# Kernel optimization log

Hardware: AMD Instinct MI355X
Metric: run time of the kernel (lower is better)

Reference implementation:

```python
import jax, jax.numpy as jnp
import numpy as np

D_MODEL, D_K, D_V = 1024, 64, 64
B, S = 4, 4096

def setup_inputs() -> dict:
    key = jax.random.key(0)
    ks = jax.random.split(key, 9)
    s_in = 1.0 / np.sqrt(D_MODEL)
    return {
        "Q": jax.random.normal(ks[0], (B, S, D_MODEL), jnp.float32),
        "K": jax.random.normal(ks[1], (B, S, D_MODEL), jnp.float32),
        "V": jax.random.normal(ks[2], (B, S, D_MODEL), jnp.float32),
        "Wq": jax.random.uniform(ks[3], (D_MODEL, D_K), jnp.float32, -s_in, s_in),
        "bq": jax.random.uniform(ks[4], (D_K,), jnp.float32, -s_in, s_in),
        "Wk": jax.random.uniform(ks[5], (D_MODEL, D_K), jnp.float32, -s_in, s_in),
        "bk": jax.random.uniform(ks[6], (D_K,), jnp.float32, -s_in, s_in),
        "Wv": jax.random.uniform(ks[7], (D_MODEL, D_V), jnp.float32, -s_in, s_in),
        "bv": jax.random.uniform(ks[8], (D_V,), jnp.float32, -s_in, s_in),
    }

def reference(Q, K, V, Wq, bq, Wk, bk, Wv, bv):
    # Linear projections: [B,S,d_model] -> [B,S,d_k/d_v]
    q = jnp.einsum("bsm,mk->bsk", Q, Wq) + bq
    k = jnp.einsum("btm,mk->btk", K, Wk) + bk
    v = jnp.einsum("btm,mv->btv", V, Wv) + bv
    # Scaled dot-product attention, softmax over key axis (dim=2)
    scores = jnp.einsum("bsk,btk->bst", q, k) / jnp.sqrt(jnp.float32(D_K))
    attn = jax.nn.softmax(scores, axis=2)  # [B,S,S]
    return jnp.einsum("bst,btv->bsv", attn, v)
```

## Files before the change

### kernel.cpp

```cpp
#include <hip/hip_runtime.h>

typedef __bf16 bf16;
typedef __attribute__((ext_vector_type(4))) __bf16 bf16x4;
typedef __attribute__((ext_vector_type(8))) __bf16 bf16x8;
typedef __attribute__((ext_vector_type(4))) float f32x4;
typedef __attribute__((ext_vector_type(16))) float f32x16;

#define MFMA16(a, b, c) __builtin_amdgcn_mfma_f32_16x16x32_bf16((a), (b), (c), 0, 0, 0)
#define MFMA32(a, b, c) __builtin_amdgcn_mfma_f32_32x32x16_bf16((a), (b), (c), 0, 0, 0)

typedef __attribute__((address_space(3))) unsigned int lds_u32_t;
typedef __attribute__((address_space(1))) unsigned int glb_u32_t;

__device__ __forceinline__ void gl2lds16(const void* g, void* l) {
    __builtin_amdgcn_global_load_lds((const glb_u32_t*)g, (lds_u32_t*)l, 16, 0, 0);
}

__device__ __forceinline__ bf16 tobf(float f) {
    unsigned u = __float_as_uint(f);
    u += 0x7fffu + ((u >> 16) & 1u);
    unsigned short h = (unsigned short)(u >> 16);
    bf16 r;
    __builtin_memcpy(&r, &h, 2);
    return r;
}

__device__ __forceinline__ bf16x8 cvt8h(f32x4 a, f32x4 b) {
    bf16x8 r;
    r[0] = (bf16)a[0]; r[1] = (bf16)a[1]; r[2] = (bf16)a[2]; r[3] = (bf16)a[3];
    r[4] = (bf16)b[0]; r[5] = (bf16)b[1]; r[6] = (bf16)b[2]; r[7] = (bf16)b[3];
    return r;
}

__global__ void wconv_kernel(const float* __restrict__ Wq, const float* __restrict__ Wk,
                             const float* __restrict__ Wv, bf16* __restrict__ Wt) {
    int j = blockIdx.y;
    const float* W = (j == 0) ? Wq : ((j == 1) ? Wk : Wv);
    int idx = blockIdx.x * 256 + threadIdx.x;
    int m = idx >> 6, n = idx & 63;
    Wt[(size_t)j * 65536 + (size_t)n * 1024 + m] = tobf(W[idx]);
}

__launch_bounds__(128, 3)
__global__ void proj_kernel(const float* __restrict__ Q, const float* __restrict__ K,
                            const float* __restrict__ V, const bf16* __restrict__ Wt,
                            const float* __restrict__ bq, const float* __restrict__ bk,
                            const float* __restrict__ bv,
                            bf16* __restrict__ q_ws, bf16* __restrict__ k_ws,
                            bf16* __restrict__ vT_ws) {
    const int j = blockIdx.y;
    const float* In   = (j == 0) ? Q : ((j == 1) ? K : V);
    const float* bias = (j == 0) ? bq : ((j == 1) ? bk : bv);
    const bf16* W = Wt + (size_t)j * 65536;

    __shared__ char smem[16384];
    char* As = smem;
    char* Bs = smem + 8192;

    const int tid = threadIdx.x;
    const int wave = tid >> 6, lane = tid & 63;
    const int quad = lane >> 4, l16 = lane & 15;
    const int rbase = blockIdx.x * 32;

    f32x4 acc[4];
#pragma unroll
    for (int nt = 0; nt < 4; nt++) acc[nt] = {0.f, 0.f, 0.f, 0.f};

    for (int kc = 0; kc < 1024; kc += 64) {
#pragma unroll
        for (int i = 0; i < 4; i++) {
            int u = i * 128 + tid;
            int row = u >> 4, cg = u & 15;
            int cgg = cg ^ (row & 15);
            gl2lds16(In + (size_t)(rbase + row) * 1024 + kc + cgg * 4,
                     As + (size_t)(i * 128 + wave * 64) * 16);
        }
#pragma unroll
        for (int i = 0; i < 4; i++) {
            int u = i * 128 + tid;
            int n = u >> 3, cg = u & 7;
            int cgg = cg ^ (n & 7);
            gl2lds16(W + (size_t)n * 1024 + kc + cgg * 8,
                     Bs + (size_t)(i * 128 + wave * 64) * 16);
        }
        __syncthreads();

        const int r = wave * 16 + l16;
#pragma unroll
        for (int p = 0; p < 2; p++) {
            int cg0 = (p * 8 + quad * 2) ^ (r & 15);
            int cg1 = (p * 8 + quad * 2 + 1) ^ (r & 15);
            f32x4 a0 = *(const f32x4*)(As + (size_t)r * 256 + cg0 * 16);
            f32x4 a1 = *(const f32x4*)(As + (size_t)r * 256 + cg1 * 16);
            bf16x8 av = cvt8h(a0, a1);
#pragma unroll
            for (int nt = 0; nt < 4; nt++) {
                int n = nt * 16 + l16;
                int cgb = (p * 4 + quad) ^ (n & 7);
                bf16x8 bv = *(const bf16x8*)(Bs + (size_t)n * 128 + cgb * 16);
                acc[nt] = MFMA16(av, bv, acc[nt]);
            }
        }
        __syncthreads();
    }

    const float scale = (j == 0) ? 0.125f * 1.44269504088896f : 1.0f;

    if (j != 2) {
        bf16* dst = (j == 0) ? q_ws : k_ws;
#pragma unroll
        for (int nt = 0; nt < 4; nt++) {
            int n = nt * 16 + l16;
            float bb = bias[n];
#pragma unroll
            for (int r4 = 0; r4 < 4; r4++) {
                int row = rbase + wave * 16 + quad * 4 + r4;
                dst[(size_t)row * 64 + n] = tobf((acc[nt][r4] + bb) * scale);
            }
        }
    } else {
        bf16 (*vtile)[40] = (bf16(*)[40])smem;
#pragma unroll
        for (int nt = 0; nt < 4; nt++) {
            int n = nt * 16 + l16;
            float bb = bias[n];
#pragma unroll
            for (int r4 = 0; r4 < 4; r4++) {
                vtile[n][wave * 16 + quad * 4 + r4] = tobf(acc[nt][r4] + bb);
            }
        }
        __syncthreads();
        int bi = rbase >> 12, t0 = rbase & 4095;
        int d = tid & 63, sel = tid >> 6;
        bf16x8 x0 = *(const bf16x8*)&vtile[d][sel * 16];
        bf16x8 x1 = *(const bf16x8*)&vtile[d][sel * 16 + 8];
        bf16* dst = vT_ws + (size_t)(bi * 64 + d) * 4096 + t0 + sel * 16;
        *(bf16x8*)dst = x0;
        *(bf16x8*)(dst + 8) = x1;
    }
}

__launch_bounds__(256, 4)
__global__ void attn_kernel(const bf16* __restrict__ q_ws, const bf16* __restrict__ k_ws,
                            const bf16* __restrict__ vT_ws,
                            float* __restrict__ po, float* __restrict__ pl,
                            float* __restrict__ out, int keys_per_split, int direct) {
    const int b = blockIdx.z, split = blockIdx.y;
    const int tid = threadIdx.x, wave = tid >> 6, lane = tid & 63;
    const int l32 = lane & 31, h = lane >> 5;
    const int sw = l32 & 7;

    __shared__ bf16 kt[64][64];
    __shared__ bf16 vt[64][64];
    __shared__ bf16 pt[4][32][64];

    const int qrow0 = b * 4096 + blockIdx.x * 128 + wave * 32;

    bf16x8 qf[4];
    const bf16* qp = q_ws + (size_t)(qrow0 + l32) * 64 + h * 8;
#pragma unroll
    for (int c = 0; c < 4; c++) qf[c] = *(const bf16x8*)(qp + c * 16);

    f32x16 o0, o1;
    float l_lane = 0.f;
#pragma unroll
    for (int i = 0; i < 16; i++) { o0[i] = 0.f; o1[i] = 0.f; }

    const int key0 = split * keys_per_split;
    const int srow = tid >> 3;
    const int sg = tid & 7;
    const int sgk = sg ^ (srow & 7);
    const bf16* kg = k_ws + (size_t)(b * 4096 + key0 + srow) * 64 + sg * 8;
    const bf16* vg = vT_ws + (size_t)(b * 64 + srow) * 4096 + key0 + sg * 8;

    uint4 kv0 = *(const uint4*)kg;
    uint4 kv1 = *(const uint4*)(kg + 2048);
    uint4 vv0 = *(const uint4*)vg;
    uint4 vv1 = *(const uint4*)(vg + 131072);

    for (int t0 = 0; t0 < keys_per_split; t0 += 64) {
        __syncthreads();
        *(uint4*)&kt[srow][sgk * 8]      = kv0;
        *(uint4*)&kt[srow + 32][sgk * 8] = kv1;
        *(uint4*)&vt[srow][sgk * 8]      = vv0;
        *(uint4*)&vt[srow + 32][sgk * 8] = vv1;
        if (t0 + 64 < keys_per_split) {
            kv0 = *(const uint4*)(kg + (size_t)(t0 + 64) * 64);
            kv1 = *(const uint4*)(kg + (size_t)(t0 + 64) * 64 + 2048);
            vv0 = *(const uint4*)(vg + t0 + 64);
            vv1 = *(const uint4*)(vg + t0 + 64 + 131072);
        }
        __syncthreads();

#pragma unroll
        for (int kt32 = 0; kt32 < 2; kt32++) {
            f32x16 s;
#pragma unroll
            for (int i = 0; i < 16; i++) s[i] = 0.f;
#pragma unroll
            for (int c = 0; c < 4; c++) {
                bf16x8 kf = *(const bf16x8*)(&kt[kt32 * 32 + l32][((2 * c + h) ^ sw) * 8]);
                s = MFMA32(kf, qf[c], s);
            }
#pragma unroll
            for (int g = 0; g < 4; g++) {
                float p0 = __builtin_amdgcn_exp2f(s[4 * g + 0]);
                float p1 = __builtin_amdgcn_exp2f(s[4 * g + 1]);
                float p2 = __builtin_amdgcn_exp2f(s[4 * g + 2]);
                float p3 = __builtin_amdgcn_exp2f(s[4 * g + 3]);
                l_lane += (p0 + p1) + (p2 + p3);
                bf16x4 pk;
                pk[0] = (bf16)p0; pk[1] = (bf16)p1; pk[2] = (bf16)p2; pk[3] = (bf16)p3;
                int gp = (kt32 * 4 + g) ^ sw;
                *(bf16x4*)(&pt[wave][l32][gp * 8 + 4 * h]) = pk;
            }
        }

#pragma unroll
        for (int tc = 0; tc < 4; tc++) {
            int gp = ((2 * tc + h) ^ sw) * 8;
            bf16x8 pf  = *(const bf16x8*)(&pt[wave][l32][gp]);
            bf16x8 vf0 = *(const bf16x8*)(&vt[l32][gp]);
            bf16x8 vf1 = *(const bf16x8*)(&vt[32 + l32][gp]);
            o0 = MFMA32(pf, vf0, o0);
            o1 = MFMA32(pf, vf1, o1);
        }
    }

    l_lane += __shfl_xor(l_lane, 32);

    if (direct) {
        float* orow = out + (size_t)qrow0 * 64;
#pragma unroll
        for (int i = 0; i < 16; i++) {
            int R = (i & 3) + 8 * (i >> 2) + 4 * h;
            float inv = 1.0f / __shfl(l_lane, R);
            orow[(size_t)R * 64 + l32]      = o0[i] * inv;
            orow[(size_t)R * 64 + 32 + l32] = o1[i] * inv;
        }
    } else {
        size_t prow = (size_t)split * 16384 + qrow0;
        float* pob = po + prow * 64;
#pragma unroll
        for (int i = 0; i < 16; i++) {
            int R = (i & 3) + 8 * (i >> 2) + 4 * h;
            pob[(size_t)R * 64 + l32]      = o0[i];
            pob[(size_t)R * 64 + 32 + l32] = o1[i];
        }
        if (h == 0) pl[prow + l32] = l_lane;
    }
}

__launch_bounds__(256)
__global__ void combine_kernel(const float* __restrict__ po, const float* __restrict__ pl,
                               float* __restrict__ out, int nsplit) {
    int idx = blockIdx.x * 256 + threadIdx.x;
    int row = idx >> 6;
    float so = 0.f, sl = 0.f;
    for (int s = 0; s < nsplit; s++) {
        so += po[(size_t)s * 1048576 + idx];
        sl += pl[(size_t)s * 16384 + row];
    }
    out[idx] = so / sl;
}

extern "C" void kernel_launch(void* const* d_in, const int* in_sizes, int n_in,
                              void* d_out, int out_size, void* d_ws, size_t ws_size,
                              hipStream_t stream) {
    const float* Q  = (const float*)d_in[0];
    const float* K  = (const float*)d_in[1];
    const float* V  = (const float*)d_in[2];
    const float* Wq = (const float*)d_in[3];
    const float* bq = (const float*)d_in[4];
    const float* Wk = (const float*)d_in[5];
    const float* bk = (const float*)d_in[6];
    const float* Wv = (const float*)d_in[7];
    const float* bv = (const float*)d_in[8];
    float* out = (float*)d_out;

    char* ws = (char*)d_ws;
    bf16* Wt    = (bf16*)ws;
    bf16* q_ws  = (bf16*)(ws + 393216);
    bf16* k_ws  = (bf16*)(ws + 393216 + 2097152);
    bf16* vT_ws = (bf16*)(ws + 393216 + 2 * 2097152);
    const size_t base = 393216 + 3 * 2097152;

    const size_t per_split = 16384u * 4u + 1048576u * 4u;
    int nsplit = 1;
    if (ws_size >= base + 8 * per_split) nsplit = 8;
    else if (ws_size >= base + 4 * per_split) nsplit = 4;
    else if (ws_size >= base + 2 * per_split) nsplit = 2;

    float* pl = (float*)(ws + base);
    float* po = (float*)(ws + base + (size_t)nsplit * 65536);

    hipLaunchKernelGGL(wconv_kernel, dim3(256, 3), dim3(256), 0, stream, Wq, Wk, Wv, Wt);
    hipLaunchKernelGGL(proj_kernel, dim3(512, 3), dim3(128), 0, stream,
                       Q, K, V, Wt, bq, bk, bv, q_ws, k_ws, vT_ws);
    hipLaunchKernelGGL(attn_kernel, dim3(32, nsplit, 4), dim3(256), 0, stream,
                       q_ws, k_ws, vT_ws, po, pl, out, 4096 / nsplit, nsplit == 1 ? 1 : 0);
    if (nsplit > 1) {
        hipLaunchKernelGGL(combine_kernel, dim3(4096), dim3(256), 0, stream, po, pl, out, nsplit);
    }
}
```

Before: 252.2 us.

## Restructure projection GEMM with register-prefetched loads and bf16 LDS staging

The projection kernel stops using direct global-to-LDS fp32 copies. Each thread now loads the fp32 input into registers, converts it to bf16 once when storing to padded LDS tiles, and prefetches the next K chunk into registers while the MFMAs run. Block size grows to 256 threads and 64 rows per block, with 128-wide K chunks, so there are fewer barriers and half the LDS traffic for A. The cost is more registers per thread, which may lower occupancy, and a simpler padding scheme in place of XOR swizzling.

```diff
diff --git a/kernel.cpp b/kernel.cpp
--- a/kernel.cpp
+++ b/kernel.cpp
@@ -8,13 +8,6 @@
 
 #define MFMA16(a, b, c) __builtin_amdgcn_mfma_f32_16x16x32_bf16((a), (b), (c), 0, 0, 0)
 #define MFMA32(a, b, c) __builtin_amdgcn_mfma_f32_32x32x16_bf16((a), (b), (c), 0, 0, 0)
-
-typedef __attribute__((address_space(3))) unsigned int lds_u32_t;
-typedef __attribute__((address_space(1))) unsigned int glb_u32_t;
-
-__device__ __forceinline__ void gl2lds16(const void* g, void* l) {
-    __builtin_amdgcn_global_load_lds((const glb_u32_t*)g, (lds_u32_t*)l, 16, 0, 0);
-}
 
 __device__ __forceinline__ bf16 tobf(float f) {
     unsigned u = __float_as_uint(f);
@@ -25,13 +18,6 @@
     return r;
 }
 
-__device__ __forceinline__ bf16x8 cvt8h(f32x4 a, f32x4 b) {
-    bf16x8 r;
-    r[0] = (bf16)a[0]; r[1] = (bf16)a[1]; r[2] = (bf16)a[2]; r[3] = (bf16)a[3];
-    r[4] = (bf16)b[0]; r[5] = (bf16)b[1]; r[6] = (bf16)b[2]; r[7] = (bf16)b[3];
-    return r;
-}
-
 __global__ void wconv_kernel(const float* __restrict__ Wq, const float* __restrict__ Wk,
                              const float* __restrict__ Wv, bf16* __restrict__ Wt) {
     int j = blockIdx.y;
@@ -41,7 +27,7 @@
     Wt[(size_t)j * 65536 + (size_t)n * 1024 + m] = tobf(W[idx]);
 }
 
-__launch_bounds__(128, 3)
+__launch_bounds__(256, 3)
 __global__ void proj_kernel(const float* __restrict__ Q, const float* __restrict__ K,
                             const float* __restrict__ V, const bf16* __restrict__ Wt,
                             const float* __restrict__ bq, const float* __restrict__ bk,
@@ -53,51 +39,70 @@
     const float* bias = (j == 0) ? bq : ((j == 1) ? bk : bv);
     const bf16* W = Wt + (size_t)j * 65536;
 
-    __shared__ char smem[16384];
-    char* As = smem;
-    char* Bs = smem + 8192;
+    __shared__ bf16 As[64][136];
+    __shared__ bf16 Bs[64][136];
 
     const int tid = threadIdx.x;
     const int wave = tid >> 6, lane = tid & 63;
     const int quad = lane >> 4, l16 = lane & 15;
-    const int rbase = blockIdx.x * 32;
+    const int rbase = blockIdx.x * 64;
+
+    int arow[8], ag[8];
+    const float* apt[8];
+#pragma unroll
+    for (int i = 0; i < 8; i++) {
+        int u = i * 256 + tid;
+        arow[i] = u >> 5; ag[i] = u & 31;
+        apt[i] = In + (size_t)(rbase + arow[i]) * 1024 + ag[i] * 4;
+    }
+    int brow[4], bg[4];
+    const bf16* bpt[4];
+#pragma unroll
+    for (int i = 0; i < 4; i++) {
+        int u = i * 256 + tid;
+        brow[i] = u >> 4; bg[i] = u & 15;
+        bpt[i] = W + (size_t)brow[i] * 1024 + bg[i] * 8;
+    }
+
+    f32x4 abuf[8];
+    bf16x8 bbuf[4];
+#pragma unroll
+    for (int i = 0; i < 8; i++) abuf[i] = *(const f32x4*)(apt[i]);
+#pragma unroll
+    for (int i = 0; i < 4; i++) bbuf[i] = *(const bf16x8*)(bpt[i]);
 
     f32x4 acc[4];
 #pragma unroll
     for (int nt = 0; nt < 4; nt++) acc[nt] = {0.f, 0.f, 0.f, 0.f};
 
-    for (int kc = 0; kc < 1024; kc += 64) {
-#pragma unroll
-        for (int i = 0; i < 4; i++) {
-            int u = i * 128 + tid;
-            int row = u >> 4, cg = u & 15;
-            int cgg = cg ^ (row & 15);
-            gl2lds16(In + (size_t)(rbase + row) * 1024 + kc + cgg * 4,
-                     As + (size_t)(i * 128 + wave * 64) * 16);
-        }
-#pragma unroll
-        for (int i = 0; i < 4; i++) {
-            int u = i * 128 + tid;
-            int n = u >> 3, cg = u & 7;
-            int cgg = cg ^ (n & 7);
-            gl2lds16(W + (size_t)n * 1024 + kc + cgg * 8,
-                     Bs + (size_t)(i * 128 + wave * 64) * 16);
+#pragma unroll
+    for (int it = 0; it < 8; it++) {
+#pragma unroll
+        for (int i = 0; i < 8; i++) {
+            bf16x4 c;
+            c[0] = (bf16)abuf[i][0]; c[1] = (bf16)abuf[i][1];
+            c[2] = (bf16)abuf[i][2]; c[3] = (bf16)abuf[i][3];
+            *(bf16x4*)&As[arow[i]][ag[i] * 4] = c;
+        }
+#pragma unroll
+        for (int i = 0; i < 4; i++) *(bf16x8*)&Bs[brow[i]][bg[i] * 8] = bbuf[i];
+
+        if (it < 7) {
+            int kn = (it + 1) * 128;
+#pragma unroll
+            for (int i = 0; i < 8; i++) abuf[i] = *(const f32x4*)(apt[i] + kn);
+#pragma unroll
+            for (int i = 0; i < 4; i++) bbuf[i] = *(const bf16x8*)(bpt[i] + kn);
         }
         __syncthreads();
 
         const int r = wave * 16 + l16;
 #pragma unroll
-        for (int p = 0; p < 2; p++) {
-            int cg0 = (p * 8 + quad * 2) ^ (r & 15);
-            int cg1 = (p * 8 + quad * 2 + 1) ^ (r & 15);
-            f32x4 a0 = *(const f32x4*)(As + (size_t)r * 256 + cg0 * 16);
-            f32x4 a1 = *(const f32x4*)(As + (size_t)r * 256 + cg1 * 16);
-            bf16x8 av = cvt8h(a0, a1);
+        for (int c = 0; c < 4; c++) {
+            bf16x8 av = *(const bf16x8*)&As[r][c * 32 + quad * 8];
 #pragma unroll
             for (int nt = 0; nt < 4; nt++) {
-                int n = nt * 16 + l16;
-                int cgb = (p * 4 + quad) ^ (n & 7);
-                bf16x8 bv = *(const bf16x8*)(Bs + (size_t)n * 128 + cgb * 16);
+                bf16x8 bv = *(const bf16x8*)&Bs[nt * 16 + l16][c * 32 + quad * 8];
                 acc[nt] = MFMA16(av, bv, acc[nt]);
             }
         }
@@ -119,7 +124,7 @@
             }
         }
     } else {
-        bf16 (*vtile)[40] = (bf16(*)[40])smem;
+        bf16 (*vtile)[72] = (bf16(*)[72])As;
 #pragma unroll
         for (int nt = 0; nt < 4; nt++) {
             int n = nt * 16 + l16;
@@ -131,10 +136,10 @@
         }
         __syncthreads();
         int bi = rbase >> 12, t0 = rbase & 4095;
-        int d = tid & 63, sel = tid >> 6;
-        bf16x8 x0 = *(const bf16x8*)&vtile[d][sel * 16];
-        bf16x8 x1 = *(const bf16x8*)&vtile[d][sel * 16 + 8];
-        bf16* dst = vT_ws + (size_t)(bi * 64 + d) * 4096 + t0 + sel * 16;
+        int d = tid >> 2, part = (tid & 3) * 16;
+        bf16x8 x0 = *(const bf16x8*)&vtile[d][part];
+        bf16x8 x1 = *(const bf16x8*)&vtile[d][part + 8];
+        bf16* dst = vT_ws + (size_t)(bi * 64 + d) * 4096 + t0 + part;
         *(bf16x8*)dst = x0;
         *(bf16x8*)(dst + 8) = x1;
     }
@@ -295,7 +300,7 @@
     float* po = (float*)(ws + base + (size_t)nsplit * 65536);
 
     hipLaunchKernelGGL(wconv_kernel, dim3(256, 3), dim3(256), 0, stream, Wq, Wk, Wv, Wt);
-    hipLaunchKernelGGL(proj_kernel, dim3(512, 3), dim3(128), 0, stream,
+    hipLaunchKernelGGL(proj_kernel, dim3(256, 3), dim3(256), 0, stream,
                        Q, K, V, Wt, bq, bk, bv, q_ws, k_ws, vT_ws);
     hipLaunchKernelGGL(attn_kernel, dim3(32, nsplit, 4), dim3(256), 0, stream,
                        q_ws, k_ws, vT_ws, po, pl, out, 4096 / nsplit, nsplit == 1 ? 1 : 0);
```

New measurement: 245.3 us. 1.03x faster.
